# Kernel optimization log

Hardware: AMD Instinct MI355X
Metric: run time of the kernel (lower is better)

The kernel has to match this reference:

```python
import jax, jax.numpy as jnp
import numpy as np

N_NODES = 50000
N_EDGES = 800000
D = 64


def setup_inputs() -> dict:
    key = jax.random.key(0)
    k1, k2, k3 = jax.random.split(key, 3)
    x = jax.random.normal(k1, (N_NODES, D), dtype=jnp.float32)
    edge_index = jax.random.randint(k2, (2, N_EDGES), 0, N_NODES, dtype=jnp.int64)
    # GCNConv linear weight (PyG stores lin.weight [out, in]; we use [in, out])
    W = jax.random.normal(k3, (D, D), dtype=jnp.float32) * (1.0 / np.sqrt(D))
    b = jnp.zeros((D,), dtype=jnp.float32)
    return {"x": x, "edge_index": edge_index, "W": W, "b": b}


def reference(x, edge_index, W, b):
    # ResidualGCNLayer forward (eval mode: dropout = identity).
    # in_channels == out_channels -> skip_connection is Identity.
    N = x.shape[0]
    E = edge_index.shape[1]
    dtype = x.dtype

    # GCNConv with add_self_loops=True, improved=False (fill value 1.0)
    loop = jnp.arange(N, dtype=edge_index.dtype)
    row = jnp.concatenate([edge_index[0], loop])  # source nodes
    col = jnp.concatenate([edge_index[1], loop])  # destination nodes
    ew = jnp.ones((E + N,), dtype=dtype)          # edge weights (self-loop fill=1)

    # symmetric normalization: D^{-1/2} A_hat D^{-1/2}
    deg = jax.ops.segment_sum(ew, col, num_segments=N)
    dinv = jnp.where(deg > 0, jax.lax.rsqrt(deg), jnp.zeros_like(deg))
    norm = dinv[row] * ew * dinv[col]             # [E+N]

    h = x @ W                                     # [N, D] transform before propagate
    msg = norm[:, None] * h[row]                  # [E+N, D] gathered + scaled messages
    agg = jax.ops.segment_sum(msg, col, num_segments=N)  # scatter-add aggregate

    identity = x                                  # Identity skip (in == out)
    out = jax.nn.relu(agg + b) + identity         # ReLU + (eval) dropout + residual
    return out
```

## Files before the change

### kernel.cpp

```cpp
#include <hip/hip_runtime.h>
#include <hip/hip_bf16.h>

#define D 64
#define CAP 64

__device__ __forceinline__ float bf16lo(unsigned u) {
    u <<= 16; return __builtin_bit_cast(float, u);
}
__device__ __forceinline__ float bf16hi(unsigned u) {
    u &= 0xffff0000u; return __builtin_bit_cast(float, u);
}
__device__ __forceinline__ unsigned bf16_rne(float f) {
    unsigned u = __builtin_bit_cast(unsigned, f);
    u += 0x7fffu + ((u >> 16) & 1u);
    return u >> 16;
}
__device__ __forceinline__ unsigned pack_bf16(float a, float b) {
    return bf16_rne(a) | (bf16_rne(b) << 16);
}

__global__ void zero_cnt_kernel(int* __restrict__ cnt, int N) {
    int i = blockIdx.x * blockDim.x + threadIdx.x;
    if (i < N) cnt[i] = 0;
}

__global__ void fill_csr_kernel(const int* __restrict__ row, const int* __restrict__ col,
                                int* __restrict__ cnt, int* __restrict__ csr, int E) {
    int e = blockIdx.x * blockDim.x + threadIdx.x;
    if (e < E) {
        int c = col[e];
        int r = row[e];
        int pos = atomicAdd(&cnt[c], 1);
        if (pos < CAP) atomicExch(&csr[c * CAP + pos], r);
    }
}

__global__ __launch_bounds__(256) void transform_kernel(
        const float* __restrict__ x, const float* __restrict__ W,
        const int* __restrict__ cnt, unsigned* __restrict__ h2b, int N) {
    __shared__ float Ws[D * D];
    __shared__ float xs[32][68];

    for (int i = threadIdx.x; i < D * D; i += 256) Ws[i] = W[i];

    const int l16 = threadIdx.x & 15;
    const int m   = threadIdx.x >> 4;
    const int base = blockIdx.x * 64;
    const float4* x4 = (const float4*)x;

    for (int pass = 0; pass < 2; ++pass) {
        int nb = base + pass * 32;
        __syncthreads();
        for (int i = threadIdx.x; i < 512; i += 256) {
            int r = i >> 4, seg = i & 15;
            int n = nb + r;
            float4 v = make_float4(0.f, 0.f, 0.f, 0.f);
            if (n < N) v = x4[n * 16 + seg];
            *(float4*)&xs[r][seg * 4] = v;
        }
        __syncthreads();

        float4 acc0 = make_float4(0.f, 0.f, 0.f, 0.f);
        float4 acc1 = make_float4(0.f, 0.f, 0.f, 0.f);
        #pragma unroll 4
        for (int k4 = 0; k4 < 16; ++k4) {
            float4 xv0 = *(const float4*)&xs[m][k4 * 4];
            float4 xv1 = *(const float4*)&xs[m + 16][k4 * 4];
            #pragma unroll
            for (int kk = 0; kk < 4; ++kk) {
                float4 w4 = *(const float4*)&Ws[(k4 * 4 + kk) * D + l16 * 4];
                float a0 = kk == 0 ? xv0.x : kk == 1 ? xv0.y : kk == 2 ? xv0.z : xv0.w;
                float a1 = kk == 0 ? xv1.x : kk == 1 ? xv1.y : kk == 2 ? xv1.z : xv1.w;
                acc0.x = fmaf(a0, w4.x, acc0.x); acc0.y = fmaf(a0, w4.y, acc0.y);
                acc0.z = fmaf(a0, w4.z, acc0.z); acc0.w = fmaf(a0, w4.w, acc0.w);
                acc1.x = fmaf(a1, w4.x, acc1.x); acc1.y = fmaf(a1, w4.y, acc1.y);
                acc1.z = fmaf(a1, w4.z, acc1.z); acc1.w = fmaf(a1, w4.w, acc1.w);
            }
        }

        int n0 = nb + m, n1 = nb + m + 16;
        if (n0 < N) {
            float dn = rsqrtf((float)(cnt[n0] + 1));
            uint2 p; p.x = pack_bf16(acc0.x * dn, acc0.y * dn);
            p.y = pack_bf16(acc0.z * dn, acc0.w * dn);
            ((uint2*)h2b)[n0 * 16 + l16] = p;
        }
        if (n1 < N) {
            float dn = rsqrtf((float)(cnt[n1] + 1));
            uint2 p; p.x = pack_bf16(acc1.x * dn, acc1.y * dn);
            p.y = pack_bf16(acc1.z * dn, acc1.w * dn);
            ((uint2*)h2b)[n1 * 16 + l16] = p;
        }
    }
}

__global__ __launch_bounds__(256) void agg_kernel(
        const float* __restrict__ x, const float* __restrict__ b,
        const unsigned* __restrict__ h2b, const int* __restrict__ cnt,
        const int* __restrict__ csr, float* __restrict__ out, int N) {
    int c = blockIdx.x * 4 + (threadIdx.x >> 6);
    if (c >= N) return;
    const int lane = threadIdx.x & 63;
    const int g = lane >> 3;
    const int l8 = lane & 7;

    const uint4* hb = (const uint4*)h2b;
    int n = cnt[c]; n = n < CAP ? n : CAP;
    const int* cb = csr + c * CAP;

    float4 accA = make_float4(0.f, 0.f, 0.f, 0.f);
    float4 accB = make_float4(0.f, 0.f, 0.f, 0.f);
    if (g == 0) {
        uint4 v = hb[c * 8 + l8];
        accA.x = bf16lo(v.x); accA.y = bf16hi(v.x);
        accA.z = bf16lo(v.y); accA.w = bf16hi(v.y);
        accB.x = bf16lo(v.z); accB.y = bf16hi(v.z);
        accB.z = bf16lo(v.w); accB.w = bf16hi(v.w);
    }

    int j = g;
    for (; j + 8 < n; j += 16) {
        int r0 = cb[j];
        int r1 = cb[j + 8];
        uint4 v0 = hb[r0 * 8 + l8];
        uint4 v1 = hb[r1 * 8 + l8];
        accA.x += bf16lo(v0.x); accA.y += bf16hi(v0.x);
        accA.z += bf16lo(v0.y); accA.w += bf16hi(v0.y);
        accB.x += bf16lo(v0.z); accB.y += bf16hi(v0.z);
        accB.z += bf16lo(v0.w); accB.w += bf16hi(v0.w);
        accA.x += bf16lo(v1.x); accA.y += bf16hi(v1.x);
        accA.z += bf16lo(v1.y); accA.w += bf16hi(v1.y);
        accB.x += bf16lo(v1.z); accB.y += bf16hi(v1.z);
        accB.z += bf16lo(v1.w); accB.w += bf16hi(v1.w);
    }
    if (j < n) {
        int r = cb[j];
        uint4 v = hb[r * 8 + l8];
        accA.x += bf16lo(v.x); accA.y += bf16hi(v.x);
        accA.z += bf16lo(v.y); accA.w += bf16hi(v.y);
        accB.x += bf16lo(v.z); accB.y += bf16hi(v.z);
        accB.z += bf16lo(v.w); accB.w += bf16hi(v.w);
    }

    #pragma unroll
    for (int mask = 8; mask <= 32; mask <<= 1) {
        accA.x += __shfl_xor(accA.x, mask); accA.y += __shfl_xor(accA.y, mask);
        accA.z += __shfl_xor(accA.z, mask); accA.w += __shfl_xor(accA.w, mask);
        accB.x += __shfl_xor(accB.x, mask); accB.y += __shfl_xor(accB.y, mask);
        accB.z += __shfl_xor(accB.z, mask); accB.w += __shfl_xor(accB.w, mask);
    }

    if (lane < 8) {
        float dc = rsqrtf((float)(cnt[c] + 1));
        float4 bv0 = ((const float4*)b)[l8 * 2];
        float4 bv1 = ((const float4*)b)[l8 * 2 + 1];
        float4 xv0 = ((const float4*)x)[c * 16 + l8 * 2];
        float4 xv1 = ((const float4*)x)[c * 16 + l8 * 2 + 1];
        float4 o0, o1;
        o0.x = fmaf(dc, accA.x, bv0.x); o0.x = o0.x > 0.f ? o0.x : 0.f; o0.x += xv0.x;
        o0.y = fmaf(dc, accA.y, bv0.y); o0.y = o0.y > 0.f ? o0.y : 0.f; o0.y += xv0.y;
        o0.z = fmaf(dc, accA.z, bv0.z); o0.z = o0.z > 0.f ? o0.z : 0.f; o0.z += xv0.z;
        o0.w = fmaf(dc, accA.w, bv0.w); o0.w = o0.w > 0.f ? o0.w : 0.f; o0.w += xv0.w;
        o1.x = fmaf(dc, accB.x, bv1.x); o1.x = o1.x > 0.f ? o1.x : 0.f; o1.x += xv1.x;
        o1.y = fmaf(dc, accB.y, bv1.y); o1.y = o1.y > 0.f ? o1.y : 0.f; o1.y += xv1.y;
        o1.z = fmaf(dc, accB.z, bv1.z); o1.z = o1.z > 0.f ? o1.z : 0.f; o1.z += xv1.z;
        o1.w = fmaf(dc, accB.w, bv1.w); o1.w = o1.w > 0.f ? o1.w : 0.f; o1.w += xv1.w;
        ((float4*)out)[c * 16 + l8 * 2]     = o0;
        ((float4*)out)[c * 16 + l8 * 2 + 1] = o1;
    }
}

extern "C" void kernel_launch(void* const* d_in, const int* in_sizes, int n_in,
                              void* d_out, int out_size, void* d_ws, size_t ws_size,
                              hipStream_t stream) {
    const float* x   = (const float*)d_in[0];
    const int*   ei  = (const int*)d_in[1];
    const float* W   = (const float*)d_in[2];
    const float* b   = (const float*)d_in[3];
    float*       out = (float*)d_out;

    const int N = in_sizes[0] / D;
    const int E = in_sizes[1] / 2;
    const int* row = ei;
    const int* col = ei + E;

    int*      cnt = (int*)d_ws;
    unsigned* h2b = (unsigned*)(cnt + N);
    int*      csr = (int*)(h2b + (size_t)N * D / 2);

    zero_cnt_kernel<<<(N + 255) / 256, 256, 0, stream>>>(cnt, N);
    fill_csr_kernel<<<(E + 255) / 256, 256, 0, stream>>>(row, col, cnt, csr, E);
    transform_kernel<<<(N + 63) / 64, 256, 0, stream>>>(x, W, cnt, h2b, N);
    agg_kernel<<<(N + 3) / 4, 256, 0, stream>>>(x, b, h2b, cnt, csr, out, N);
}
```

Measured before the change: 181.2 us.

## Fuse CSR fill with feature transform and move source-degree scaling into aggregation

Result: faster. 167.0 us (-7.9%).

```diff
diff --git a/kernel.cpp b/kernel.cpp
--- a/kernel.cpp
+++ b/kernel.cpp
@@ -24,22 +24,24 @@
     if (i < N) cnt[i] = 0;
 }
 
-__global__ void fill_csr_kernel(const int* __restrict__ row, const int* __restrict__ col,
-                                int* __restrict__ cnt, int* __restrict__ csr, int E) {
-    int e = blockIdx.x * blockDim.x + threadIdx.x;
-    if (e < E) {
-        int c = col[e];
-        int r = row[e];
-        int pos = atomicAdd(&cnt[c], 1);
-        if (pos < CAP) atomicExch(&csr[c * CAP + pos], r);
-    }
-}
-
-__global__ __launch_bounds__(256) void transform_kernel(
+__global__ __launch_bounds__(256) void fused_fill_transform_kernel(
         const float* __restrict__ x, const float* __restrict__ W,
-        const int* __restrict__ cnt, unsigned* __restrict__ h2b, int N) {
+        const int* __restrict__ row, const int* __restrict__ col,
+        int* __restrict__ cnt, int* __restrict__ csr,
+        unsigned* __restrict__ h2b, int N, int E, int trBlocks) {
     __shared__ float Ws[D * D];
     __shared__ float xs[32][68];
+
+    if (blockIdx.x >= trBlocks) {
+        int e = (blockIdx.x - trBlocks) * 256 + threadIdx.x;
+        if (e < E) {
+            int c = col[e];
+            int r = row[e];
+            int pos = atomicAdd(&cnt[c], 1);
+            if (pos < CAP) atomicExch(&csr[c * CAP + pos], r);
+        }
+        return;
+    }
 
     for (int i = threadIdx.x; i < D * D; i += 256) Ws[i] = W[i];
 
@@ -80,15 +82,13 @@
 
         int n0 = nb + m, n1 = nb + m + 16;
         if (n0 < N) {
-            float dn = rsqrtf((float)(cnt[n0] + 1));
-            uint2 p; p.x = pack_bf16(acc0.x * dn, acc0.y * dn);
-            p.y = pack_bf16(acc0.z * dn, acc0.w * dn);
+            uint2 p; p.x = pack_bf16(acc0.x, acc0.y);
+            p.y = pack_bf16(acc0.z, acc0.w);
             ((uint2*)h2b)[n0 * 16 + l16] = p;
         }
         if (n1 < N) {
-            float dn = rsqrtf((float)(cnt[n1] + 1));
-            uint2 p; p.x = pack_bf16(acc1.x * dn, acc1.y * dn);
-            p.y = pack_bf16(acc1.z * dn, acc1.w * dn);
+            uint2 p; p.x = pack_bf16(acc1.x, acc1.y);
+            p.y = pack_bf16(acc1.z, acc1.w);
             ((uint2*)h2b)[n1 * 16 + l16] = p;
         }
     }
@@ -105,41 +105,46 @@
     const int l8 = lane & 7;
 
     const uint4* hb = (const uint4*)h2b;
-    int n = cnt[c]; n = n < CAP ? n : CAP;
+    const int deg = cnt[c];
+    const float dc = rsqrtf((float)(deg + 1));
+    int n = deg < CAP ? deg : CAP;
     const int* cb = csr + c * CAP;
 
     float4 accA = make_float4(0.f, 0.f, 0.f, 0.f);
     float4 accB = make_float4(0.f, 0.f, 0.f, 0.f);
     if (g == 0) {
         uint4 v = hb[c * 8 + l8];
-        accA.x = bf16lo(v.x); accA.y = bf16hi(v.x);
-        accA.z = bf16lo(v.y); accA.w = bf16hi(v.y);
-        accB.x = bf16lo(v.z); accB.y = bf16hi(v.z);
-        accB.z = bf16lo(v.w); accB.w = bf16hi(v.w);
+        accA.x = dc * bf16lo(v.x); accA.y = dc * bf16hi(v.x);
+        accA.z = dc * bf16lo(v.y); accA.w = dc * bf16hi(v.y);
+        accB.x = dc * bf16lo(v.z); accB.y = dc * bf16hi(v.z);
+        accB.z = dc * bf16lo(v.w); accB.w = dc * bf16hi(v.w);
     }
 
     int j = g;
     for (; j + 8 < n; j += 16) {
         int r0 = cb[j];
         int r1 = cb[j + 8];
+        float d0 = rsqrtf((float)(cnt[r0] + 1));
+        float d1 = rsqrtf((float)(cnt[r1] + 1));
         uint4 v0 = hb[r0 * 8 + l8];
         uint4 v1 = hb[r1 * 8 + l8];
-        accA.x += bf16lo(v0.x); accA.y += bf16hi(v0.x);
-        accA.z += bf16lo(v0.y); accA.w += bf16hi(v0.y);
-        accB.x += bf16lo(v0.z); accB.y += bf16hi(v0.z);
-        accB.z += bf16lo(v0.w); accB.w += bf16hi(v0.w);
-        accA.x += bf16lo(v1.x); accA.y += bf16hi(v1.x);
-        accA.z += bf16lo(v1.y); accA.w += bf16hi(v1.y);
-        accB.x += bf16lo(v1.z); accB.y += bf16hi(v1.z);
-        accB.z += bf16lo(v1.w); accB.w += bf16hi(v1.w);
+        accA.x = fmaf(d0, bf16lo(v0.x), accA.x); accA.y = fmaf(d0, bf16hi(v0.x), accA.y);
+        accA.z = fmaf(d0, bf16lo(v0.y), accA.z); accA.w = fmaf(d0, bf16hi(v0.y), accA.w);
+        accB.x = fmaf(d0, bf16lo(v0.z), accB.x); accB.y = fmaf(d0, bf16hi(v0.z), accB.y);
+        accB.z = fmaf(d0, bf16lo(v0.w), accB.z); accB.w = fmaf(d0, bf16hi(v0.w), accB.w);
+        accA.x = fmaf(d1, bf16lo(v1.x), accA.x); accA.y = fmaf(d1, bf16hi(v1.x), accA.y);
+        accA.z = fmaf(d1, bf16lo(v1.y), accA.z); accA.w = fmaf(d1, bf16hi(v1.y), accA.w);
+        accB.x = fmaf(d1, bf16lo(v1.z), accB.x); accB.y = fmaf(d1, bf16hi(v1.z), accB.y);
+        accB.z = fmaf(d1, bf16lo(v1.w), accB.z); accB.w = fmaf(d1, bf16hi(v1.w), accB.w);
     }
     if (j < n) {
         int r = cb[j];
+        float dr = rsqrtf((float)(cnt[r] + 1));
         uint4 v = hb[r * 8 + l8];
-        accA.x += bf16lo(v.x); accA.y += bf16hi(v.x);
-        accA.z += bf16lo(v.y); accA.w += bf16hi(v.y);
-        accB.x += bf16lo(v.z); accB.y += bf16hi(v.z);
-        accB.z += bf16lo(v.w); accB.w += bf16hi(v.w);
+        accA.x = fmaf(dr, bf16lo(v.x), accA.x); accA.y = fmaf(dr, bf16hi(v.x), accA.y);
+        accA.z = fmaf(dr, bf16lo(v.y), accA.z); accA.w = fmaf(dr, bf16hi(v.y), accA.w);
+        accB.x = fmaf(dr, bf16lo(v.z), accB.x); accB.y = fmaf(dr, bf16hi(v.z), accB.y);
+        accB.z = fmaf(dr, bf16lo(v.w), accB.z); accB.w = fmaf(dr, bf16hi(v.w), accB.w);
     }
 
     #pragma unroll
@@ -151,7 +156,6 @@
     }
 
     if (lane < 8) {
-        float dc = rsqrtf((float)(cnt[c] + 1));
         float4 bv0 = ((const float4*)b)[l8 * 2];
         float4 bv1 = ((const float4*)b)[l8 * 2 + 1];
         float4 xv0 = ((const float4*)x)[c * 16 + l8 * 2];
@@ -188,8 +192,11 @@
     unsigned* h2b = (unsigned*)(cnt + N);
     int*      csr = (int*)(h2b + (size_t)N * D / 2);
 
+    const int trBlocks   = (N + 63) / 64;
+    const int fillBlocks = (E + 255) / 256;
+
     zero_cnt_kernel<<<(N + 255) / 256, 256, 0, stream>>>(cnt, N);
-    fill_csr_kernel<<<(E + 255) / 256, 256, 0, stream>>>(row, col, cnt, csr, E);
-    transform_kernel<<<(N + 63) / 64, 256, 0, stream>>>(x, W, cnt, h2b, N);
+    fused_fill_transform_kernel<<<trBlocks + fillBlocks, 256, 0, stream>>>(
+        x, W, row, col, cnt, csr, h2b, N, E, trBlocks);
     agg_kernel<<<(N + 3) / 4, 256, 0, stream>>>(x, b, h2b, cnt, csr, out, N);
 }
```
